# Kernel optimization log

Measured on AMD Instinct MI355X. Metric: run time of the kernel, lower is better.

The kernel has to match this reference:

```python
import math
import jax, jax.numpy as jnp
import numpy as np

MODEL_DIM = 2048
NUM_EXPERTS = 64
NUM_TOKENS = 8192
CAPACITY_FACTOR = 1.0


def setup_inputs() -> dict:
    key = jax.random.key(0)
    kx, kw = jax.random.split(key)
    x = jax.random.normal(kx, (NUM_TOKENS, MODEL_DIM), dtype=jnp.float32)
    # Linear(model_dim, num_experts, bias=False): weight [E, D], y = x @ W.T
    wg = jax.random.normal(kw, (NUM_EXPERTS, MODEL_DIM), dtype=jnp.float32) * (1.0 / math.sqrt(MODEL_DIM))
    return {"x": x, "wg": wg}


def reference(x, wg):
    # ---- gate projection: logits [S, E] ----
    logits = jnp.einsum('sd,ed->se', x, wg)
    gates = jax.nn.softmax(logits, axis=1)
    S, E = gates.shape
    # training mode -> capacity = capacity_factor * ceil(S / E)  (static)
    capacity = int(CAPACITY_FACTOR * math.ceil(S / E))

    # ---- top-1 expert selection ----
    indices1_s = jnp.argmax(gates, axis=1)                      # [S]
    mask1 = jax.nn.one_hot(indices1_s, E, dtype=jnp.int32)      # [S, E]

    # gate value of the chosen expert per token
    gates1_s = jnp.sum(gates * mask1.astype(gates.dtype), axis=1)  # [S]

    # position of each token within its expert's queue (cumsum over tokens)
    locations1 = jnp.cumsum(mask1, axis=0) - 1                  # [S, E]

    # ---- load-balancing auxiliary loss ----
    me = jnp.mean(gates, axis=0)                                # [E]
    ce = jnp.mean(mask1.astype(gates.dtype), axis=0)            # [E]
    l_aux = jnp.mean(me * ce) * (E * E)

    # ---- capacity enforcement: drop tokens beyond expert capacity ----
    mask1 = mask1 * (locations1 < capacity).astype(mask1.dtype) # [S, E]
    locations1_s = jnp.sum(locations1 * mask1, axis=1)          # [S]

    # ---- combine / dispatch tensors ----
    gates1 = gates1_s[:, None] * mask1.astype(gates.dtype)      # [S, E]
    locations1_sc = jax.nn.one_hot(locations1_s, capacity, dtype=gates.dtype)  # [S, C]
    # torch.bmm(gates1[:, :, None], locations1_sc[:, None, :]) == outer product per token
    combine1_sec = jnp.einsum('se,sc->sec', gates1, locations1_sc)  # [S, E, C]
    dispatch_mask = combine1_sec > 0                            # bool [S, E, C]

    return l_aux, combine1_sec, dispatch_mask
```

## Files before the change

### kernel.cpp

```cpp
#include <hip/hip_runtime.h>
#include <math.h>

#define DIM     2048
#define NEXP    64
#define CAP     128
#define NTOK    8192
#define NTILE   256
#define KC      256
#define NCH     (DIM/KC)
#define XWSTR   260
#define PSTR    68
#define RF      67108864
#define FBLK    4096
#define FCH     8192

typedef float vfloat4 __attribute__((ext_vector_type(4)));

__global__ __launch_bounds__(256) void fill(float* __restrict__ out)
{
    vfloat4* o4 = reinterpret_cast<vfloat4*>(out);
    const vfloat4 z4 = {0.f, 0.f, 0.f, 0.f};
    const size_t base = (size_t)blockIdx.x * FCH + threadIdx.x;
    #pragma unroll
    for (int k = 0; k < 32; ++k)
        o4[base + (size_t)(k << 8)] = z4;
    if (blockIdx.x == 0 && threadIdx.x == 0)
        out[134217728ull] = 0.0f;
}

__global__ __launch_bounds__(512, 2) void gate(
    const float* __restrict__ x, const float* __restrict__ wg,
    int* __restrict__ expert_idx, float* __restrict__ gate_top,
    int* __restrict__ rank,
    float* __restrict__ me_partial, int* __restrict__ counts)
{
    __shared__ __align__(16) float smem[(32 + NEXP) * XWSTR];
    __shared__ float me_w[8 * NEXP];
    __shared__ int   cnt_w[8 * NEXP];
    __shared__ int   exp_s[32];

    float* xs = smem;
    float* ws = smem + 32 * XWSTR;

    const int tid  = threadIdx.x;
    const int gb   = blockIdx.x;
    const int tok0 = gb * 32;
    const int sl   = tid >> 5;
    const int i    = tid & 31;
    const int tg   = i & 3;
    const int eg   = i >> 2;
    const int kb   = sl * 16;

    float acc[8][8] = {};

    for (int ch = 0; ch < NCH; ++ch) {
        const int k0 = ch * KC;
        #pragma unroll
        for (int q = 0; q < 4; ++q) {
            int id = tid + (q << 9);
            int r = id >> 6, c = id & 63;
            float4 v = *(const float4*)(x + (size_t)(tok0 + r) * DIM + k0 + 4 * c);
            *(float4*)(&xs[r * XWSTR + 4 * c]) = v;
        }
        #pragma unroll
        for (int q = 0; q < 8; ++q) {
            int id = tid + (q << 9);
            int r = id >> 6, c = id & 63;
            float4 v = *(const float4*)(wg + (size_t)r * DIM + k0 + 4 * c);
            *(float4*)(&ws[r * XWSTR + 4 * c]) = v;
        }
        __syncthreads();

        #pragma unroll
        for (int q2 = 0; q2 < 4; ++q2) {
            const int kk = kb + 4 * q2;
            float4 xt[8], we[8];
            #pragma unroll
            for (int j = 0; j < 8; ++j)
                xt[j] = *(const float4*)(&xs[(tg + 4 * j) * XWSTR + kk]);
            #pragma unroll
            for (int m = 0; m < 8; ++m)
                we[m] = *(const float4*)(&ws[(eg + 8 * m) * XWSTR + kk]);
            #pragma unroll
            for (int j = 0; j < 8; ++j)
                #pragma unroll
                for (int m = 0; m < 8; ++m) {
                    acc[j][m] = fmaf(xt[j].x, we[m].x, acc[j][m]);
                    acc[j][m] = fmaf(xt[j].y, we[m].y, acc[j][m]);
                    acc[j][m] = fmaf(xt[j].z, we[m].z, acc[j][m]);
                    acc[j][m] = fmaf(xt[j].w, we[m].w, acc[j][m]);
                }
        }
        __syncthreads();
    }

    float* part = smem;
    float* lgt  = smem + 8 * 32 * PSTR;
    if (sl >= 8) {
        #pragma unroll
        for (int j = 0; j < 8; ++j)
            #pragma unroll
            for (int m = 0; m < 8; ++m)
                part[((sl - 8) * 32 + tg + 4 * j) * PSTR + eg + 8 * m] = acc[j][m];
    }
    __syncthreads();
    if (sl < 8) {
        #pragma unroll
        for (int j = 0; j < 8; ++j)
            #pragma unroll
            for (int m = 0; m < 8; ++m) {
                int idx = (sl * 32 + tg + 4 * j) * PSTR + eg + 8 * m;
                part[idx] += acc[j][m];
            }
    }
    __syncthreads();

    {
        int t  = tid >> 4;
        int e0 = (tid & 15) << 2;
        float4 a = {0, 0, 0, 0};
        #pragma unroll
        for (int s2 = 0; s2 < 8; ++s2) {
            float4 p = *(const float4*)(&part[(s2 * 32 + t) * PSTR + e0]);
            a.x += p.x; a.y += p.y; a.z += p.z; a.w += p.w;
        }
        *(float4*)(&lgt[t * PSTR + e0]) = a;
    }
    __syncthreads();

    const int lane = tid & 63;
    const int wv   = tid >> 6;
    float me_acc  = 0.0f;
    int   cnt_acc = 0;
    #pragma unroll
    for (int r4 = 0; r4 < 4; ++r4) {
        int row = wv * 4 + r4;
        float v = lgt[row * PSTR + lane];
        float m = v; int mi = lane;
        #pragma unroll
        for (int off = 32; off > 0; off >>= 1) {
            float om  = __shfl_xor(m, off);
            int   omi = __shfl_xor(mi, off);
            if (om > m || (om == m && omi < mi)) { m = om; mi = omi; }
        }
        float ex = __expf(v - m);
        float sm = ex;
        #pragma unroll
        for (int off = 32; off > 0; off >>= 1) sm += __shfl_xor(sm, off);
        me_acc += ex / sm;
        if (lane == mi) {
            expert_idx[tok0 + row] = mi;
            gate_top[tok0 + row]   = 1.0f / sm;
            exp_s[row] = mi;
            ++cnt_acc;
        }
    }
    me_w[wv * NEXP + lane]  = me_acc;
    cnt_w[wv * NEXP + lane] = cnt_acc;
    __syncthreads();

    if (tid < 32) {
        int e = exp_s[tid];
        int rk = 0;
        for (int u = 0; u < tid; ++u) rk += (exp_s[u] == e) ? 1 : 0;
        rank[tok0 + tid] = rk;
    }
    if (tid < NEXP) {
        float ms = 0.f; int cs = 0;
        #pragma unroll
        for (int w = 0; w < 8; ++w) { ms += me_w[w * NEXP + tid]; cs += cnt_w[w * NEXP + tid]; }
        me_partial[gb * NEXP + tid] = ms;
        counts[gb * NEXP + tid]     = cs;
    }
}

__global__ __launch_bounds__(1024) void prefix_pos(
    const float* __restrict__ me_partial, const int* __restrict__ counts,
    const int* __restrict__ expert_idx, const int* __restrict__ rank,
    int* __restrict__ pos_g, float* __restrict__ laux)
{
    __shared__ int   bo_l[NTILE * NEXP];
    __shared__ int   cnt_l[16 * NEXP];
    __shared__ float me_l[16 * NEXP];
    __shared__ int   cnt_tot[NEXP];
    __shared__ float me_tot[NEXP];

    const int tid = threadIdx.x;
    const int e   = tid & 63;
    const int g   = tid >> 6;

    int cs = 0; float ms = 0.f;
    #pragma unroll
    for (int i = 0; i < 16; ++i) {
        int t = g * 16 + i;
        cs += counts[t * NEXP + e];
        ms += me_partial[t * NEXP + e];
    }
    cnt_l[g * NEXP + e] = cs;
    me_l[g * NEXP + e]  = ms;
    __syncthreads();

    if (g == 0) {
        int run = 0; float mt = 0.f;
        #pragma unroll
        for (int i = 0; i < 16; ++i) {
            int c = cnt_l[i * NEXP + e];
            cnt_l[i * NEXP + e] = run;
            run += c;
            mt  += me_l[i * NEXP + e];
        }
        cnt_tot[e] = run;
        me_tot[e]  = mt;
    }
    __syncthreads();

    int run = cnt_l[g * NEXP + e];
    #pragma unroll
    for (int i = 0; i < 16; ++i) {
        int t = g * 16 + i;
        bo_l[t * NEXP + e] = run;
        run += counts[t * NEXP + e];
    }
    __syncthreads();

    if (tid < NEXP) {
        float v = (me_tot[e] / (float)NTOK) * ((float)cnt_tot[e] / (float)NTOK);
        #pragma unroll
        for (int off = 32; off > 0; off >>= 1) v += __shfl_xor(v, off);
        if (e == 0) laux[0] = v * (float)NEXP;
    }

    #pragma unroll
    for (int ii = 0; ii < 8; ++ii) {
        int s  = tid + (ii << 10);
        int ex = expert_idx[s];
        int loc = bo_l[(s >> 5) * NEXP + ex] + rank[s];
        pos_g[s] = (loc < CAP) ? (1 + s * (NEXP * CAP) + ex * CAP + loc) : -1;
    }
}

__global__ __launch_bounds__(64) void patch(
    const int* __restrict__ pos_g, const float* __restrict__ gate_top,
    const float* __restrict__ laux, float* __restrict__ out)
{
    const int s = blockIdx.x * 64 + threadIdx.x;
    const int p = pos_g[s];
    if (p >= 0) {
        out[(size_t)p]      = gate_top[s];
        out[(size_t)p + RF] = 1.0f;
    }
    if (s == 0) out[0] = laux[0];
}

extern "C" void kernel_launch(void* const* d_in, const int* in_sizes, int n_in,
                              void* d_out, int out_size, void* d_ws, size_t ws_size,
                              hipStream_t stream)
{
    const float* x  = (const float*)d_in[0];
    const float* wg = (const float*)d_in[1];
    float* out = (float*)d_out;

    char* ws = (char*)d_ws;
    int*   expert_idx = (int*)  (ws);
    float* gate_top   = (float*)(ws + 32768);
    int*   rank       = (int*)  (ws + 65536);
    float* me_partial = (float*)(ws + 98304);
    int*   counts     = (int*)  (ws + 163840);
    int*   pos_g      = (int*)  (ws + 229376);
    float* laux       = (float*)(ws + 262144);

    fill<<<FBLK, 256, 0, stream>>>(out);
    gate<<<NTILE, 512, 0, stream>>>(x, wg, expert_idx, gate_top, rank,
                                    me_partial, counts);
    prefix_pos<<<1, 1024, 0, stream>>>(me_partial, counts, expert_idx, rank,
                                       pos_g, laux);
    patch<<<128, 64, 0, stream>>>(pos_g, gate_top, laux, out);
}
```

Before: 612.3 us.

## Fuse output zero-fill into gate GEMM kernel with nontemporal stores

Removes the standalone fill kernel and has each gate block zero its slice of the large output buffer inside the K-chunk loop, using nontemporal stores placed between the global loads and the LDS writes. The goal is to overlap the roughly half-gigabyte write of zeros with the gate GEMM compute and drop one launch. It also replaces __syncthreads with explicit lgkmcnt waits and s_barrier fenced by sched_barrier, so outstanding global stores are not waited on at each barrier. The trade-off is that the GEMM now competes with heavy store traffic, and the sched_barrier fences restrict the compiler's instruction scheduling.

```diff
diff --git a/kernel.cpp b/kernel.cpp
--- a/kernel.cpp
+++ b/kernel.cpp
@@ -11,25 +11,12 @@
 #define XWSTR   260
 #define PSTR    68
 #define RF      67108864
-#define FBLK    4096
-#define FCH     8192
 
 typedef float vfloat4 __attribute__((ext_vector_type(4)));
 
-__global__ __launch_bounds__(256) void fill(float* __restrict__ out)
-{
-    vfloat4* o4 = reinterpret_cast<vfloat4*>(out);
-    const vfloat4 z4 = {0.f, 0.f, 0.f, 0.f};
-    const size_t base = (size_t)blockIdx.x * FCH + threadIdx.x;
-    #pragma unroll
-    for (int k = 0; k < 32; ++k)
-        o4[base + (size_t)(k << 8)] = z4;
-    if (blockIdx.x == 0 && threadIdx.x == 0)
-        out[134217728ull] = 0.0f;
-}
-
-__global__ __launch_bounds__(512, 2) void gate(
+__global__ __launch_bounds__(512, 2) void gate_fill(
     const float* __restrict__ x, const float* __restrict__ wg,
+    float* __restrict__ out,
     int* __restrict__ expert_idx, float* __restrict__ gate_top,
     int* __restrict__ rank,
     float* __restrict__ me_partial, int* __restrict__ counts)
@@ -51,25 +38,51 @@
     const int eg   = i >> 2;
     const int kb   = sl * 16;
 
+    vfloat4* o4 = reinterpret_cast<vfloat4*>(out);
+    const vfloat4 z4 = {0.f, 0.f, 0.f, 0.f};
+    if (gb == 0 && tid == 0)
+        out[134217728ull] = 0.0f;
+
     float acc[8][8] = {};
 
     for (int ch = 0; ch < NCH; ++ch) {
         const int k0 = ch * KC;
+        float4 xv[4], wv[8];
         #pragma unroll
         for (int q = 0; q < 4; ++q) {
             int id = tid + (q << 9);
             int r = id >> 6, c = id & 63;
-            float4 v = *(const float4*)(x + (size_t)(tok0 + r) * DIM + k0 + 4 * c);
-            *(float4*)(&xs[r * XWSTR + 4 * c]) = v;
+            xv[q] = *(const float4*)(x + (size_t)(tok0 + r) * DIM + k0 + 4 * c);
         }
         #pragma unroll
         for (int q = 0; q < 8; ++q) {
             int id = tid + (q << 9);
             int r = id >> 6, c = id & 63;
-            float4 v = *(const float4*)(wg + (size_t)r * DIM + k0 + 4 * c);
-            *(float4*)(&ws[r * XWSTR + 4 * c]) = v;
-        }
-        __syncthreads();
+            wv[q] = *(const float4*)(wg + (size_t)r * DIM + k0 + 4 * c);
+        }
+        {
+            size_t base = (size_t)gb * 131072 + (size_t)(ch << 14) + tid;
+            #pragma unroll
+            for (int k = 0; k < 32; ++k)
+                __builtin_nontemporal_store(z4, &o4[base + (size_t)(k << 9)]);
+        }
+        #pragma unroll
+        for (int q = 0; q < 4; ++q) {
+            int id = tid + (q << 9);
+            int r = id >> 6, c = id & 63;
+            *(float4*)(&xs[r * XWSTR + 4 * c]) = xv[q];
+        }
+        #pragma unroll
+        for (int q = 0; q < 8; ++q) {
+            int id = tid + (q << 9);
+            int r = id >> 6, c = id & 63;
+            *(float4*)(&ws[r * XWSTR + 4 * c]) = wv[q];
+        }
+        __builtin_amdgcn_sched_barrier(0);
+        asm volatile("s_waitcnt lgkmcnt(0)" ::: "memory");
+        __builtin_amdgcn_sched_barrier(0);
+        __builtin_amdgcn_s_barrier();
+        __builtin_amdgcn_sched_barrier(0);
 
         #pragma unroll
         for (int q2 = 0; q2 < 4; ++q2) {
@@ -91,7 +104,12 @@
                     acc[j][m] = fmaf(xt[j].w, we[m].w, acc[j][m]);
                 }
         }
-        __syncthreads();
+
+        __builtin_amdgcn_sched_barrier(0);
+        asm volatile("s_waitcnt lgkmcnt(0)" ::: "memory");
+        __builtin_amdgcn_sched_barrier(0);
+        __builtin_amdgcn_s_barrier();
+        __builtin_amdgcn_sched_barrier(0);
     }
 
     float* part = smem;
@@ -129,12 +147,12 @@
     __syncthreads();
 
     const int lane = tid & 63;
-    const int wv   = tid >> 6;
+    const int wv2  = tid >> 6;
     float me_acc  = 0.0f;
     int   cnt_acc = 0;
     #pragma unroll
     for (int r4 = 0; r4 < 4; ++r4) {
-        int row = wv * 4 + r4;
+        int row = wv2 * 4 + r4;
         float v = lgt[row * PSTR + lane];
         float m = v; int mi = lane;
         #pragma unroll
@@ -155,8 +173,8 @@
             ++cnt_acc;
         }
     }
-    me_w[wv * NEXP + lane]  = me_acc;
-    cnt_w[wv * NEXP + lane] = cnt_acc;
+    me_w[wv2 * NEXP + lane]  = me_acc;
+    cnt_w[wv2 * NEXP + lane] = cnt_acc;
     __syncthreads();
 
     if (tid < 32) {
@@ -269,9 +287,8 @@
     int*   pos_g      = (int*)  (ws + 229376);
     float* laux       = (float*)(ws + 262144);
 
-    fill<<<FBLK, 256, 0, stream>>>(out);
-    gate<<<NTILE, 512, 0, stream>>>(x, wg, expert_idx, gate_top, rank,
-                                    me_partial, counts);
+    gate_fill<<<NTILE, 512, 0, stream>>>(x, wg, out, expert_idx, gate_top,
+                                         rank, me_partial, counts);
     prefix_pos<<<1, 1024, 0, stream>>>(me_partial, counts, expert_idx, rank,
                                        pos_g, laux);
     patch<<<128, 64, 0, stream>>>(pos_g, gate_top, laux, out);
```

Result: no change. 606.2 us (-1.0%).
